# Kernel tuning notes

Hardware: AMD Instinct MI355X
Metric: run time of the kernel (lower is better)

The kernel has to match this reference:

```python
import jax, jax.numpy as jnp
import numpy as np

IN_FEATURES = 2048
OUT_FEATURES = 256
KERNEL_DIMS = 8
BATCH = 256


def setup_inputs() -> dict:
    key = jax.random.key(0)
    k_x, k_T = jax.random.split(key)
    x = jax.random.normal(k_x, (BATCH, IN_FEATURES), dtype=jnp.float32)
    # nn.Parameter(torch.randn(in, out, kd)) with normal_(0, 1) init
    T = jax.random.normal(k_T, (IN_FEATURES, OUT_FEATURES, KERNEL_DIMS), dtype=jnp.float32)
    return {"x": x, "T": T}


def reference(x, T):
    # M: [B, out_features, kernel_dims]
    M = jnp.einsum('bi,iok->bok', x, T)
    # Pairwise L1 distance over kernel dims: norm[i, j, o] = sum_k |M[j,o,k] - M[i,o,k]|
    # (matches torch M.unsqueeze(0) - M.permute(1,0,2,3); abs makes order irrelevant)
    norm = jnp.abs(M[None, :, :, :] - M[:, None, :, :]).sum(axis=3)  # [B, B, out]
    o_b = jnp.exp(-norm).sum(axis=0) - 1.0  # subtract self-similarity exp(0)=1
    return jnp.concatenate([x, o_b], axis=1)  # [B, in_features + out_features]
```

## Files before the change

kernel.cpp:

```cpp
#include <hip/hip_runtime.h>
#include <math.h>

#define BATCH   256
#define IN_F    2048
#define OUT_F   256
#define NCOL    2048
#define OSTRIDE 2304
#define LOG2E   1.4426950408889634f

typedef float    f32x4  __attribute__((ext_vector_type(4)));
typedef short    bf16x8 __attribute__((ext_vector_type(8)));
typedef _Float16 h16x2  __attribute__((ext_vector_type(2)));
typedef __fp16   fp16x2 __attribute__((ext_vector_type(2)));
typedef unsigned short u16;
typedef unsigned int   u32;

#define WT_BASE   (16u << 20)
#define XB_BASE   (64u << 20)

__device__ __forceinline__ u16 f2bf(float f) {
    unsigned u = __builtin_bit_cast(unsigned, f);
    u += 0x7fff + ((u >> 16) & 1);
    return (u16)(u >> 16);
}

__device__ __forceinline__ float exp2_fast(float x) {
#if __has_builtin(__builtin_amdgcn_exp2f)
    return __builtin_amdgcn_exp2f(x);
#else
    float r; asm("v_exp_f32 %0, %1" : "=v"(r) : "v"(x)); return r;
#endif
}

__device__ __forceinline__ float hsum_neg(h16x2 s) {
#if __has_builtin(__builtin_amdgcn_fdot2)
    const h16x2 n1 = {(_Float16)-1.0f, (_Float16)-1.0f};
    return __builtin_amdgcn_fdot2(s, n1, 0.0f, false);
#else
    return -((float)s[0] + (float)s[1]);
#endif
}

__device__ __forceinline__ float bperm(int srcLane, float v) {
    return __builtin_bit_cast(float,
        __builtin_amdgcn_ds_bpermute(srcLane * 4, __builtin_bit_cast(int, v)));
}

__global__ __launch_bounds__(256)
void k_prep(const float* __restrict__ X, const float* __restrict__ T,
            u16* __restrict__ Wt, u16* __restrict__ Xb,
            float* __restrict__ out) {
    const int b = blockIdx.x, t = threadIdx.x;
    if (b < 128) {
        const int c8 = b & 7;
        const int kg = b >> 3;
        const int p  = t & 127;
        const int C  = c8 + 8 * (p >> 4);
        const int n  = C * 32 + (p & 15) * 2;
        const int kh = (t >> 7) * 64;
        const int nt = n >> 4, n16 = n & 15;
#pragma unroll
        for (int kc = 0; kc < 8; ++kc) {
            const int kb = kg * 128 + kh + kc * 8;
            u16 h0[8], h1[8];
#pragma unroll
            for (int r = 0; r < 8; ++r) {
                float2 v = *(const float2*)(T + (size_t)(kb + r) * NCOL + n);
                h0[r] = f2bf(v.x);
                h1[r] = f2bf(v.y);
            }
            u16* dst = Wt + ((size_t)(nt * 256 + (kb >> 3)) * 16 + n16) * 8;
            *(float4*)dst       = *(float4*)h0;
            *(float4*)(dst + 8) = *(float4*)h1;
        }
    } else {
        const int g   = b - 128;
        const int rt  = g >> 4;
        const int kc  = (g & 15) * 16 + (t & 15);
        const int r16 = t >> 4;
        const int row = rt * 16 + r16;
        const float* src = X + (size_t)row * IN_F + kc * 8;
        float4 v0 = *(const float4*)src;
        float4 v1 = *(const float4*)(src + 4);
        u16 h[8] = {f2bf(v0.x * LOG2E), f2bf(v0.y * LOG2E),
                    f2bf(v0.z * LOG2E), f2bf(v0.w * LOG2E),
                    f2bf(v1.x * LOG2E), f2bf(v1.y * LOG2E),
                    f2bf(v1.z * LOG2E), f2bf(v1.w * LOG2E)};
        *(float4*)(Xb + ((size_t)(rt * 256 + kc) * 16 + r16) * 8) = *(float4*)h;
        float* od = out + (size_t)row * OSTRIDE + kc * 8;
        *(float4*)od       = v0;
        *(float4*)(od + 4) = v1;
    }
}

__global__ __launch_bounds__(512, 4)
void k_gemm(const u16* __restrict__ Xb, const u16* __restrict__ Wt,
            u16* __restrict__ Mh) {
    __shared__ float L[8][32][33];
    const int t = threadIdx.x, l = t & 63, kcw = t >> 6;
    const int bid = blockIdx.x;
    const int R = bid >> 6;
    const int C = bid & 63;

    const int lo = (l >> 4) * 128 + (l & 15) * 8;
    const u16* ap0 = Xb + (size_t)(R * 2) * 32768 + kcw * 4096 + lo;
    const u16* ap1 = ap0 + 32768;
    const u16* bp0 = Wt + (size_t)(C * 2) * 32768 + kcw * 4096 + lo;
    const u16* bp1 = bp0 + 32768;

    f32x4 c00 = {0.f,0.f,0.f,0.f}, c01 = {0.f,0.f,0.f,0.f};
    f32x4 c10 = {0.f,0.f,0.f,0.f}, c11 = {0.f,0.f,0.f,0.f};

#pragma unroll 8
    for (int s = 0; s < 8; ++s) {
        bf16x8 a0 = *(const bf16x8*)(ap0 + s * 512);
        bf16x8 a1 = *(const bf16x8*)(ap1 + s * 512);
        bf16x8 b0 = *(const bf16x8*)(bp0 + s * 512);
        bf16x8 b1 = *(const bf16x8*)(bp1 + s * 512);
        c00 = __builtin_amdgcn_mfma_f32_16x16x32_bf16(a0, b0, c00, 0, 0, 0);
        c01 = __builtin_amdgcn_mfma_f32_16x16x32_bf16(a0, b1, c01, 0, 0, 0);
        c10 = __builtin_amdgcn_mfma_f32_16x16x32_bf16(a1, b0, c10, 0, 0, 0);
        c11 = __builtin_amdgcn_mfma_f32_16x16x32_bf16(a1, b1, c11, 0, 0, 0);
    }

    const int lq = l >> 4, lm = l & 15;
#define PUT(acc, qi, qj) do { \
        _Pragma("unroll") \
        for (int r = 0; r < 4; ++r) \
            L[kcw][(qj) * 16 + lm][(qi) * 16 + lq * 4 + r] = acc[r]; \
    } while (0)
    PUT(c00, 0, 0); PUT(c01, 0, 1); PUT(c10, 1, 0); PUT(c11, 1, 1);
#undef PUT
    __syncthreads();

    if (t < 256) {
        const int o2 = t >> 6;
        const int jl = (t & 63) >> 1;
        const int k0 = (t & 1) * 4;
        float v[4];
#pragma unroll
        for (int i = 0; i < 4; ++i) {
            const int c = o2 * 8 + k0 + i;
            float s0 = (L[0][c][jl] + L[1][c][jl]) + (L[2][c][jl] + L[3][c][jl]);
            float s1 = (L[4][c][jl] + L[5][c][jl]) + (L[6][c][jl] + L[7][c][jl]);
            v[i] = s0 + s1;
        }
        fp16x2 p0 = __builtin_amdgcn_cvt_pkrtz(v[0], v[1]);
        fp16x2 p1 = __builtin_amdgcn_cvt_pkrtz(v[2], v[3]);
        uint2 pk = {__builtin_bit_cast(u32, p0), __builtin_bit_cast(u32, p1)};
        *(uint2*)(Mh + ((size_t)(C * 4 + o2) * 256 + R * 32 + jl) * 8 + k0) = pk;
    }
}

__global__ __launch_bounds__(1024)
void k_pair(const u16* __restrict__ Mh, float* __restrict__ out) {
    __shared__ __align__(16) uint4 Msh[BATCH];
    __shared__ float Ps[16][256];
    const int t = threadIdx.x;
    const int g = blockIdx.x & 7, idx = blockIdx.x >> 3;
    const int o = (g + 8 * (idx >> 2)) * 4 + (idx & 3);

    if (t < 256) Msh[t] = ((const uint4*)(Mh + (size_t)o * 2048))[t];
    __syncthreads();

    const int jg = t & 63, q = t >> 6;
    h16x2 m[4][4];
#pragma unroll
    for (int c = 0; c < 4; ++c) {
        uint4 mm = Msh[jg + 64 * c];
        m[c][0] = __builtin_bit_cast(h16x2, mm.x);
        m[c][1] = __builtin_bit_cast(h16x2, mm.y);
        m[c][2] = __builtin_bit_cast(h16x2, mm.z);
        m[c][3] = __builtin_bit_cast(h16x2, mm.w);
    }

    float acc[4] = {0.f, 0.f, 0.f, 0.f};
    const int dbase = q * 8 + 1;
#pragma unroll
    for (int ii = 0; ii < 8; ++ii) {
        const int d  = dbase + ii;
        const int dd = d & 63;
        const int dl = d >> 6;
        float e[4];
#pragma unroll
        for (int c = 0; c < 4; ++c) {
            uint4 uu = Msh[(jg + 64 * c + d) & 255];
            h16x2 d0 = __builtin_bit_cast(h16x2, uu.x) - m[c][0];
            h16x2 d1 = __builtin_bit_cast(h16x2, uu.y) - m[c][1];
            h16x2 d2 = __builtin_bit_cast(h16x2, uu.z) - m[c][2];
            h16x2 d3 = __builtin_bit_cast(h16x2, uu.w) - m[c][3];
            h16x2 e0 = __builtin_bit_cast(h16x2, __builtin_bit_cast(u32, d0) & 0x7fff7fffu);
            h16x2 e1 = __builtin_bit_cast(h16x2, __builtin_bit_cast(u32, d1) & 0x7fff7fffu);
            h16x2 e2 = __builtin_bit_cast(h16x2, __builtin_bit_cast(u32, d2) & 0x7fff7fffu);
            h16x2 e3 = __builtin_bit_cast(h16x2, __builtin_bit_cast(u32, d3) & 0x7fff7fffu);
            h16x2 s = (e0 + e1) + (e2 + e3);
            float ev = exp2_fast(hsum_neg(s));
            e[c] = ev;
            acc[c] += ev;
        }
        if (d != 128) {
            const int src = (jg - dd) & 63;
            float r0 = bperm(src, e[0]);
            float r1 = bperm(src, e[1]);
            float r2 = bperm(src, e[2]);
            float r3 = bperm(src, e[3]);
            const int rot = dl + (jg < dd ? 1 : 0);
            acc[0] += rot == 0 ? r0 : (rot == 1 ? r3 : r2);
            acc[1] += rot == 0 ? r1 : (rot == 1 ? r0 : r3);
            acc[2] += rot == 0 ? r2 : (rot == 1 ? r1 : r0);
            acc[3] += rot == 0 ? r3 : (rot == 1 ? r2 : r1);
        }
    }
#pragma unroll
    for (int c = 0; c < 4; ++c) Ps[q][jg + 64 * c] = acc[c];
    __syncthreads();

    if (t < 256) {
        float s = 0.f;
#pragma unroll
        for (int q2 = 0; q2 < 16; ++q2) s += Ps[q2][t];
        out[(size_t)t * OSTRIDE + IN_F + o] = s;
    }
}

extern "C" void kernel_launch(void* const* d_in, const int* in_sizes, int n_in,
                              void* d_out, int out_size, void* d_ws, size_t ws_size,
                              hipStream_t stream) {
    const float* x = (const float*)d_in[0];
    const float* T = (const float*)d_in[1];
    float* out = (float*)d_out;
    char* ws = (char*)d_ws;
    u16* Mh = (u16*)ws;
    u16* Wt = (u16*)(ws + WT_BASE);
    u16* Xb = (u16*)(ws + XB_BASE);

    k_prep<<<384, 256, 0, stream>>>(x, T, Wt, Xb, out);
    k_gemm<<<512, 512, 0, stream>>>(Xb, Wt, Mh);
    k_pair<<<256, 1024, 0, stream>>>(Mh, out);
}
```

Baseline: 26.20 us.

## Replicate bf16 X per XCD and split the passthrough copy into separate blocks

k_prep now writes eight copies of the bf16-converted, log2e-scaled X matrix, one per block group selected by blockIdx&7. k_gemm reads the copy matching its bid&7, so blocks likely scheduled on the same XCD share a local L2-resident copy instead of pulling a single copy across dies. The fp32 passthrough of x into the output moves into 128 dedicated blocks, and the launch grows to 512 blocks. This costs eight times the Xb write traffic (about 8 MB total) in exchange for GEMM A-operand reads that should stay local to each XCD's L2.

```diff
diff --git a/kernel.cpp b/kernel.cpp
--- a/kernel.cpp
+++ b/kernel.cpp
@@ -17,6 +17,7 @@
 
 #define WT_BASE   (16u << 20)
 #define XB_BASE   (64u << 20)
+#define XB_COPY   524288u
 
 __device__ __forceinline__ u16 f2bf(float f) {
     unsigned u = __builtin_bit_cast(unsigned, f);
@@ -73,23 +74,37 @@
             *(float4*)dst       = *(float4*)h0;
             *(float4*)(dst + 8) = *(float4*)h1;
         }
+    } else if (b < 384) {
+        const int g    = b & 7;
+        const int idx  = (b - 128) >> 3;
+        const int rt   = idx >> 1;
+        const int half = idx & 1;
+        const int r16  = t >> 4;
+        const int kcq  = t & 15;
+        const int row  = rt * 16 + r16;
+        u16* XbL = Xb + (size_t)g * XB_COPY;
+#pragma unroll
+        for (int kk = 0; kk < 8; ++kk) {
+            const int kc = half * 128 + kk * 16 + kcq;
+            const float* src = X + (size_t)row * IN_F + kc * 8;
+            float4 v0 = *(const float4*)src;
+            float4 v1 = *(const float4*)(src + 4);
+            u16 h[8] = {f2bf(v0.x * LOG2E), f2bf(v0.y * LOG2E),
+                        f2bf(v0.z * LOG2E), f2bf(v0.w * LOG2E),
+                        f2bf(v1.x * LOG2E), f2bf(v1.y * LOG2E),
+                        f2bf(v1.z * LOG2E), f2bf(v1.w * LOG2E)};
+            *(float4*)(XbL + ((size_t)(rt * 256 + kc) * 16 + r16) * 8) =
+                *(float4*)h;
+        }
     } else {
-        const int g   = b - 128;
-        const int rt  = g >> 4;
-        const int kc  = (g & 15) * 16 + (t & 15);
-        const int r16 = t >> 4;
-        const int row = rt * 16 + r16;
-        const float* src = X + (size_t)row * IN_F + kc * 8;
-        float4 v0 = *(const float4*)src;
-        float4 v1 = *(const float4*)(src + 4);
-        u16 h[8] = {f2bf(v0.x * LOG2E), f2bf(v0.y * LOG2E),
-                    f2bf(v0.z * LOG2E), f2bf(v0.w * LOG2E),
-                    f2bf(v1.x * LOG2E), f2bf(v1.y * LOG2E),
-                    f2bf(v1.z * LOG2E), f2bf(v1.w * LOG2E)};
-        *(float4*)(Xb + ((size_t)(rt * 256 + kc) * 16 + r16) * 8) = *(float4*)h;
-        float* od = out + (size_t)row * OSTRIDE + kc * 8;
-        *(float4*)od       = v0;
-        *(float4*)(od + 4) = v1;
+        const int g2  = b - 384;
+        const int row = g2 * 2 + (t >> 7);
+        const int c0  = (t & 127) * 16;
+        const float* src = X + (size_t)row * IN_F + c0;
+        float* dst = out + (size_t)row * OSTRIDE + c0;
+#pragma unroll
+        for (int i = 0; i < 4; ++i)
+            *(float4*)(dst + i * 4) = *(const float4*)(src + i * 4);
     }
 }
 
@@ -102,8 +117,9 @@
     const int R = bid >> 6;
     const int C = bid & 63;
 
+    const u16* XbL = Xb + (size_t)(bid & 7) * XB_COPY;
     const int lo = (l >> 4) * 128 + (l & 15) * 8;
-    const u16* ap0 = Xb + (size_t)(R * 2) * 32768 + kcw * 4096 + lo;
+    const u16* ap0 = XbL + (size_t)(R * 2) * 32768 + kcw * 4096 + lo;
     const u16* ap1 = ap0 + 32768;
     const u16* bp0 = Wt + (size_t)(C * 2) * 32768 + kcw * 4096 + lo;
     const u16* bp1 = bp0 + 32768;
@@ -234,7 +250,7 @@
     u16* Wt = (u16*)(ws + WT_BASE);
     u16* Xb = (u16*)(ws + XB_BASE);
 
-    k_prep<<<384, 256, 0, stream>>>(x, T, Wt, Xb, out);
+    k_prep<<<512, 256, 0, stream>>>(x, T, Wt, Xb, out);
     k_gemm<<<512, 512, 0, stream>>>(Xb, Wt, Mh);
     k_pair<<<256, 1024, 0, stream>>>(Mh, out);
 }
```

Result: slower. 29.63 us (+13.1%).

## Switch GEMM operands to FP8 and move x copy into pair kernel

Applied to the files above, without the earlier changes.

Quantizes x (pre-scaled by log2e) and T to FP8 instead of BF16 and uses the fp8 16x16x32 MFMA in the GEMM. This halves the operand bytes written by prep and read by the GEMM. The prep kernel now uses half as many x blocks, and the copy of x into the output moves into the pairwise kernel, one row per block. FP8 precision is much coarser, so the L1 distances and exp sums could fall outside tolerance.

```diff
diff --git a/kernel.cpp b/kernel.cpp
--- a/kernel.cpp
+++ b/kernel.cpp
@@ -9,20 +9,15 @@
 #define LOG2E   1.4426950408889634f
 
 typedef float    f32x4  __attribute__((ext_vector_type(4)));
-typedef short    bf16x8 __attribute__((ext_vector_type(8)));
 typedef _Float16 h16x2  __attribute__((ext_vector_type(2)));
 typedef __fp16   fp16x2 __attribute__((ext_vector_type(2)));
 typedef unsigned short u16;
 typedef unsigned int   u32;
+typedef unsigned char  u8;
+typedef long long      i64;
 
 #define WT_BASE   (16u << 20)
-#define XB_BASE   (64u << 20)
-
-__device__ __forceinline__ u16 f2bf(float f) {
-    unsigned u = __builtin_bit_cast(unsigned, f);
-    u += 0x7fff + ((u >> 16) & 1);
-    return (u16)(u >> 16);
-}
+#define XB_BASE   (24u << 20)
 
 __device__ __forceinline__ float exp2_fast(float x) {
 #if __has_builtin(__builtin_amdgcn_exp2f)
@@ -46,10 +41,16 @@
         __builtin_amdgcn_ds_bpermute(srcLane * 4, __builtin_bit_cast(int, v)));
 }
 
+__device__ __forceinline__ u32 pk4_fp8(float a, float b, float c, float d) {
+    u32 r;
+    asm("v_cvt_pk_fp8_f32 %0, %1, %2" : "=v"(r) : "v"(a), "v"(b));
+    asm("v_cvt_pk_fp8_f32 %0, %1, %2 op_sel:[0,0,1]" : "+v"(r) : "v"(c), "v"(d));
+    return r;
+}
+
 __global__ __launch_bounds__(256)
 void k_prep(const float* __restrict__ X, const float* __restrict__ T,
-            u16* __restrict__ Wt, u16* __restrict__ Xb,
-            float* __restrict__ out) {
+            u8* __restrict__ Wt, u8* __restrict__ Xb) {
     const int b = blockIdx.x, t = threadIdx.x;
     if (b < 128) {
         const int c8 = b & 7;
@@ -62,39 +63,44 @@
 #pragma unroll
         for (int kc = 0; kc < 8; ++kc) {
             const int kb = kg * 128 + kh + kc * 8;
-            u16 h0[8], h1[8];
+            float a0[8], a1[8];
 #pragma unroll
             for (int r = 0; r < 8; ++r) {
                 float2 v = *(const float2*)(T + (size_t)(kb + r) * NCOL + n);
-                h0[r] = f2bf(v.x);
-                h1[r] = f2bf(v.y);
+                a0[r] = v.x;
+                a1[r] = v.y;
             }
-            u16* dst = Wt + ((size_t)(nt * 256 + (kb >> 3)) * 16 + n16) * 8;
-            *(float4*)dst       = *(float4*)h0;
-            *(float4*)(dst + 8) = *(float4*)h1;
+            uint2 p0 = {pk4_fp8(a0[0], a0[1], a0[2], a0[3]),
+                        pk4_fp8(a0[4], a0[5], a0[6], a0[7])};
+            uint2 p1 = {pk4_fp8(a1[0], a1[1], a1[2], a1[3]),
+                        pk4_fp8(a1[4], a1[5], a1[6], a1[7])};
+            u8* dst = Wt + ((size_t)(nt * 256 + (kb >> 3)) * 16 + n16) * 8;
+            *(uint2*)dst       = p0;
+            *(uint2*)(dst + 8) = p1;
         }
     } else {
         const int g   = b - 128;
-        const int rt  = g >> 4;
-        const int kc  = (g & 15) * 16 + (t & 15);
+        const int rt  = g >> 3;
+        const int kcb = (g & 7) * 32;
         const int r16 = t >> 4;
+        const int kc  = kcb + (t & 15) * 2;
         const int row = rt * 16 + r16;
         const float* src = X + (size_t)row * IN_F + kc * 8;
-        float4 v0 = *(const float4*)src;
-        float4 v1 = *(const float4*)(src + 4);
-        u16 h[8] = {f2bf(v0.x * LOG2E), f2bf(v0.y * LOG2E),
-                    f2bf(v0.z * LOG2E), f2bf(v0.w * LOG2E),
-                    f2bf(v1.x * LOG2E), f2bf(v1.y * LOG2E),
-                    f2bf(v1.z * LOG2E), f2bf(v1.w * LOG2E)};
-        *(float4*)(Xb + ((size_t)(rt * 256 + kc) * 16 + r16) * 8) = *(float4*)h;
-        float* od = out + (size_t)row * OSTRIDE + kc * 8;
-        *(float4*)od       = v0;
-        *(float4*)(od + 4) = v1;
+        float v[16];
+#pragma unroll
+        for (int i = 0; i < 4; ++i)
+            *(f32x4*)(v + i * 4) = *(const f32x4*)(src + i * 4);
+        uint2 q0 = {pk4_fp8(v[0] * LOG2E, v[1] * LOG2E, v[2] * LOG2E, v[3] * LOG2E),
+                    pk4_fp8(v[4] * LOG2E, v[5] * LOG2E, v[6] * LOG2E, v[7] * LOG2E)};
+        uint2 q1 = {pk4_fp8(v[8] * LOG2E, v[9] * LOG2E, v[10] * LOG2E, v[11] * LOG2E),
+                    pk4_fp8(v[12] * LOG2E, v[13] * LOG2E, v[14] * LOG2E, v[15] * LOG2E)};
+        *(uint2*)(Xb + ((size_t)(rt * 256 + kc)     * 16 + r16) * 8) = q0;
+        *(uint2*)(Xb + ((size_t)(rt * 256 + kc + 1) * 16 + r16) * 8) = q1;
     }
 }
 
 __global__ __launch_bounds__(512, 4)
-void k_gemm(const u16* __restrict__ Xb, const u16* __restrict__ Wt,
+void k_gemm(const u8* __restrict__ Xb, const u8* __restrict__ Wt,
             u16* __restrict__ Mh) {
     __shared__ float L[8][32][33];
     const int t = threadIdx.x, l = t & 63, kcw = t >> 6;
@@ -103,24 +109,24 @@
     const int C = bid & 63;
 
     const int lo = (l >> 4) * 128 + (l & 15) * 8;
-    const u16* ap0 = Xb + (size_t)(R * 2) * 32768 + kcw * 4096 + lo;
-    const u16* ap1 = ap0 + 32768;
-    const u16* bp0 = Wt + (size_t)(C * 2) * 32768 + kcw * 4096 + lo;
-    const u16* bp1 = bp0 + 32768;
+    const u8* ap0 = Xb + (size_t)(R * 2) * 32768 + kcw * 4096 + lo;
+    const u8* ap1 = ap0 + 32768;
+    const u8* bp0 = Wt + (size_t)(C * 2) * 32768 + kcw * 4096 + lo;
+    const u8* bp1 = bp0 + 32768;
 
     f32x4 c00 = {0.f,0.f,0.f,0.f}, c01 = {0.f,0.f,0.f,0.f};
     f32x4 c10 = {0.f,0.f,0.f,0.f}, c11 = {0.f,0.f,0.f,0.f};
 
 #pragma unroll 8
     for (int s = 0; s < 8; ++s) {
-        bf16x8 a0 = *(const bf16x8*)(ap0 + s * 512);
-        bf16x8 a1 = *(const bf16x8*)(ap1 + s * 512);
-        bf16x8 b0 = *(const bf16x8*)(bp0 + s * 512);
-        bf16x8 b1 = *(const bf16x8*)(bp1 + s * 512);
-        c00 = __builtin_amdgcn_mfma_f32_16x16x32_bf16(a0, b0, c00, 0, 0, 0);
-        c01 = __builtin_amdgcn_mfma_f32_16x16x32_bf16(a0, b1, c01, 0, 0, 0);
-        c10 = __builtin_amdgcn_mfma_f32_16x16x32_bf16(a1, b0, c10, 0, 0, 0);
-        c11 = __builtin_amdgcn_mfma_f32_16x16x32_bf16(a1, b1, c11, 0, 0, 0);
+        i64 a0 = *(const i64*)(ap0 + s * 512);
+        i64 a1 = *(const i64*)(ap1 + s * 512);
+        i64 b0 = *(const i64*)(bp0 + s * 512);
+        i64 b1 = *(const i64*)(bp1 + s * 512);
+        c00 = __builtin_amdgcn_mfma_f32_16x16x32_fp8_fp8(a0, b0, c00, 0, 0, 0);
+        c01 = __builtin_amdgcn_mfma_f32_16x16x32_fp8_fp8(a0, b1, c01, 0, 0, 0);
+        c10 = __builtin_amdgcn_mfma_f32_16x16x32_fp8_fp8(a1, b0, c10, 0, 0, 0);
+        c11 = __builtin_amdgcn_mfma_f32_16x16x32_fp8_fp8(a1, b1, c11, 0, 0, 0);
     }
 
     const int lq = l >> 4, lm = l & 15;
@@ -153,7 +159,8 @@
 }
 
 __global__ __launch_bounds__(1024)
-void k_pair(const u16* __restrict__ Mh, float* __restrict__ out) {
+void k_pair(const u16* __restrict__ Mh, const float* __restrict__ X,
+            float* __restrict__ out) {
     __shared__ __align__(16) uint4 Msh[BATCH];
     __shared__ float Ps[16][256];
     const int t = threadIdx.x;
@@ -161,6 +168,12 @@
     const int o = (g + 8 * (idx >> 2)) * 4 + (idx & 3);
 
     if (t < 256) Msh[t] = ((const uint4*)(Mh + (size_t)o * 2048))[t];
+
+    {
+        const int row = blockIdx.x;
+        *(float2*)(out + (size_t)row * OSTRIDE + t * 2) =
+            *(const float2*)(X + (size_t)row * IN_F + t * 2);
+    }
     __syncthreads();
 
     const int jg = t & 63, q = t >> 6;
@@ -231,10 +244,10 @@
     float* out = (float*)d_out;
     char* ws = (char*)d_ws;
     u16* Mh = (u16*)ws;
-    u16* Wt = (u16*)(ws + WT_BASE);
-    u16* Xb = (u16*)(ws + XB_BASE);
-
-    k_prep<<<384, 256, 0, stream>>>(x, T, Wt, Xb, out);
+    u8*  Wt = (u8*)(ws + WT_BASE);
+    u8*  Xb = (u8*)(ws + XB_BASE);
+
+    k_prep<<<256, 256, 0, stream>>>(x, T, Wt, Xb);
     k_gemm<<<512, 512, 0, stream>>>(Xb, Wt, Mh);
-    k_pair<<<256, 1024, 0, stream>>>(Mh, out);
-}
+    k_pair<<<256, 1024, 0, stream>>>(Mh, x, out);
+}
```

After: 23.52 us (median of 2 runs). -10.2%, faster.
